# Performance work log

Measured on AMD Instinct MI355X. Metric: run time of the kernel, lower is better.

## Reference

```python
import jax, jax.numpy as jnp
import numpy as np

N = 20000
E = 640000
F_IN = 128
C_T = 8
L_T = 10 * N
HEADS = 8
HDIM = 64
NEG_SLOPE = 0.2


def setup_inputs() -> dict:
    key = jax.random.key(0)
    ks = jax.random.split(key, 20)
    d = {}
    d["x"] = jax.random.normal(ks[0], (N, F_IN), dtype=jnp.float32)
    d["edge_index"] = jax.random.randint(ks[1], (2, E), 0, N, dtype=jnp.int64)
    d["temporal"] = jax.random.normal(ks[2], (C_T, L_T), dtype=jnp.float32)
    # GCNConv(F_IN, 16)
    d["W1"] = jax.random.normal(ks[3], (F_IN, 16), dtype=jnp.float32) * 0.1
    d["b1"] = jnp.zeros((16,), dtype=jnp.float32)
    # GATConv(16, 64, heads=8), concat -> 512
    d["W2"] = jax.random.normal(ks[4], (16, HEADS * HDIM), dtype=jnp.float32) * 0.1
    d["att_src"] = jax.random.normal(ks[5], (HEADS, HDIM), dtype=jnp.float32) * 0.1
    d["att_dst"] = jax.random.normal(ks[6], (HEADS, HDIM), dtype=jnp.float32) * 0.1
    d["b2"] = jnp.zeros((HEADS * HDIM,), dtype=jnp.float32)
    # TemporalCNN
    d["cw1"] = jax.random.normal(ks[7], (32, C_T, 3), dtype=jnp.float32) * 0.1
    d["cb1"] = jnp.zeros((32,), dtype=jnp.float32)
    d["cw2"] = jax.random.normal(ks[8], (64, 32, 3), dtype=jnp.float32) * 0.05
    d["cb2"] = jnp.zeros((64,), dtype=jnp.float32)
    d["cw3"] = jax.random.normal(ks[9], (128, 64, 3), dtype=jnp.float32) * 0.05
    d["cb3"] = jnp.zeros((128,), dtype=jnp.float32)
    d["fw1"] = jax.random.normal(ks[10], (256, 128 * 10), dtype=jnp.float32) * 0.02
    d["fb1"] = jnp.zeros((256,), dtype=jnp.float32)
    d["fw2"] = jax.random.normal(ks[11], (64, 256), dtype=jnp.float32) * 0.05
    d["fb2"] = jnp.zeros((64,), dtype=jnp.float32)
    return d


def _conv1d(x, w, b):
    # x: [1, C, L], w: [O, C, 3]; padding=1 == SAME for k=3
    out = jax.lax.conv_general_dilated(
        x, w, window_strides=(1,), padding="SAME",
        dimension_numbers=("NCH", "OIH", "NCH"))
    return out + b[None, :, None]


def _gcn(x, src, dst, W, b):
    # PyG GCNConv: add self-loops, symmetric normalization
    h = x @ W                                   # [N, 16]
    deg = jax.ops.segment_sum(jnp.ones_like(dst, dtype=h.dtype), dst, num_segments=N)
    dinv = jax.lax.rsqrt(jnp.maximum(deg, 1.0))
    norm = dinv[src] * dinv[dst]                # [E+N]
    out = jax.ops.segment_sum(h[src] * norm[:, None], dst, num_segments=N)
    return out + b


def _gat(x, src, dst, W, att_src, att_dst, b):
    h = (x @ W).reshape(N, HEADS, HDIM)         # [N, 8, 64]
    a_s = jnp.einsum("nhd,hd->nh", h, att_src)  # [N, 8]
    a_d = jnp.einsum("nhd,hd->nh", h, att_dst)
    e = a_s[src] + a_d[dst]                     # [E+N, 8], message j->i: src=j, dst=i
    e = jnp.where(e >= 0, e, NEG_SLOPE * e)     # LeakyReLU(0.2)
    # segment softmax over incoming edges of each dst node
    m = jax.ops.segment_max(e, dst, num_segments=N)
    m = jnp.where(jnp.isfinite(m), m, 0.0)
    ex = jnp.exp(e - m[dst])
    s = jax.ops.segment_sum(ex, dst, num_segments=N)
    alpha = ex / (s[dst] + 1e-16)               # [E+N, 8]
    out = jax.ops.segment_sum(h[src] * alpha[:, :, None], dst, num_segments=N)
    return out.reshape(N, HEADS * HDIM) + b


def reference(x, edge_index, temporal, W1, b1, W2, att_src, att_dst, b2,
              cw1, cb1, cw2, cb2, cw3, cb3, fw1, fb1, fw2, fb2):
    # ---- graph branch ----
    loops = jnp.arange(N, dtype=edge_index.dtype)
    src = jnp.concatenate([edge_index[0], loops])
    dst = jnp.concatenate([edge_index[1], loops])
    g = _gcn(x, src, dst, W1, b1)
    g = jax.nn.relu(g)
    # F.dropout with training=False (eval) -> identity
    x1 = _gat(g, src, dst, W2, att_src, att_dst, b2)   # [N, 512]
    # ---- temporal branch ----
    t = temporal[None]                                  # [1, C, L]
    t = jax.nn.relu(_conv1d(t, cw1, cb1))
    t = jax.nn.relu(_conv1d(t, cw2, cb2))
    t = jax.nn.relu(_conv1d(t, cw3, cb3))               # [1, 128, L]
    t = t.reshape(-1, 128 * 10)                         # [N, 1280] (same as torch .view)
    t = jax.nn.relu(t @ fw1.T + fb1)
    x2 = t @ fw2.T + fb2                                # [N, 64]
    return jnp.concatenate([x1, x2], axis=1)            # [N, 576]
```

## Files before the change

### kernel.cpp

```cpp
#include <hip/hip_runtime.h>
#include <hip/hip_bf16.h>

#define NN 20000
#define EE 640000
#define FIN 128
#define CT 8
#define LT 200000
#define HEADS 8
#define HDIM 64
#define F1 16
#define F2 512
#define OUTF 576

typedef short s16x8 __attribute__((ext_vector_type(8)));
typedef float f32x4 __attribute__((ext_vector_type(4)));

static __device__ __forceinline__ float b2f(__hip_bfloat16 v) { return __bfloat162float(v); }
static __device__ __forceinline__ float ldf(float v) { return v; }
static __device__ __forceinline__ float ldf(__hip_bfloat16 v) { return __bfloat162float(v); }
static __device__ __forceinline__ unsigned f2bf_bits(float x) {
  unsigned u = __float_as_uint(x);
  return (u + 0x7fffu + ((u >> 16) & 1u)) >> 16;
}

static __device__ __forceinline__ void gl16(const void* g, void* l) {
  __builtin_amdgcn_global_load_lds(
      (const __attribute__((address_space(1))) unsigned*)g,
      (__attribute__((address_space(3))) unsigned*)l, 16, 0, 0);
}

__global__ __launch_bounds__(256) void prep_all(
    const float* __restrict__ cw1, float* __restrict__ wt1,
    const float* __restrict__ cw2, short* __restrict__ wb2,
    const float* __restrict__ cw3, short* __restrict__ wb3,
    const float* __restrict__ W2, const float* __restrict__ asrc,
    const float* __restrict__ adst, float* __restrict__ WS, float* __restrict__ WD) {
  int b = blockIdx.x, t = threadIdx.x;
  if (b < 3) {
    int i = b * 256 + t;
    if (i < 32 * 8 * 3) {
      int o = i / 24, r = i % 24;
      int c = r / 3, k = r % 3;
      wt1[(c * 3 + k) * 32 + o] = cw1[i];
    }
  } else if (b < 27) {
    int i = (b - 3) * 256 + t;
    int o = i / 96, r = i % 96;
    int ic = r / 3, kk = r % 3;
    wb2[o * 96 + kk * 32 + ic] = (short)f2bf_bits(cw2[i]);
  } else if (b < 123) {
    int i = (b - 27) * 256 + t;
    int o = i / 192, r = i % 192;
    int ic = r / 3, kk = r % 3;
    wb3[o * 192 + kk * 64 + ic] = (short)f2bf_bits(cw3[i]);
  } else {
    int k = (t & 127) >> 3, h = t & 7;
    const float* av = (t < 128) ? asrc : adst;
    float acc = 0.f;
    for (int d = 0; d < 64; d++) acc += W2[k * F2 + h * 64 + d] * av[h * 64 + d];
    ((t < 128) ? WS : WD)[k * 8 + h] = acc;
  }
}

__global__ __launch_bounds__(256) void fwprep(
    const float* __restrict__ fw1, __hip_bfloat16* __restrict__ w1b,
    const float* __restrict__ fw2, float* __restrict__ fw2t) {
  int b = blockIdx.x;
  if (b < 1280) {
    int i = b * 256 + threadIdx.x;
    w1b[i] = __float2bfloat16(fw1[i]);
  } else {
    int i = (b - 1280) * 256 + threadIdx.x;
    int o = i / 256, j = i % 256;
    fw2t[j * 64 + o] = fw2[i];
  }
}


template <int C, int O, int P, typename IN_T>
__global__ __launch_bounds__(256) void conv_fast(
    const IN_T* __restrict__ in, __hip_bfloat16* __restrict__ out,
    const float* __restrict__ wt, const float* __restrict__ bias) {
  constexpr int OCG = O / 2;
  constexpr int PG = 256 / OCG;
  static_assert(PG * P == 64, "tile mismatch");
  __shared__ __align__(16) float tile[C][68];
  __shared__ __align__(16) __hip_bfloat16 ot[O][66];
  int t = threadIdx.x;
  int ocg = t % OCG;
  int pg = t / OCG;
  long base = (long)blockIdx.x * 64;

  for (int i = t; i < C * 66; i += 256) {
    int c = i / 66, p = i % 66;
    long l = base + p - 1;
    tile[c][p] = (l >= 0 && l < LT) ? ldf(in[(long)c * LT + l]) : 0.f;
  }
  __syncthreads();

  int oc0 = 2 * ocg;
  int p0 = pg * P;
  float acc[2][P];
#pragma unroll
  for (int j = 0; j < 2; j++)
#pragma unroll
    for (int p = 0; p < P; p++) acc[j][p] = 0.f;

  for (int ic = 0; ic < C; ic++) {
    float x[P + 2];
#pragma unroll
    for (int q = 0; q < P / 4; q++) {
      float4 v = *(const float4*)&tile[ic][p0 + 4 * q];
      x[4 * q] = v.x; x[4 * q + 1] = v.y; x[4 * q + 2] = v.z; x[4 * q + 3] = v.w;
    }
    {
      float2 v = *(const float2*)&tile[ic][p0 + P];
      x[P] = v.x; x[P + 1] = v.y;
    }
    const float* wrow = wt + (long)ic * 3 * O;
    float wv[3][2];
#pragma unroll
    for (int kk = 0; kk < 3; kk++) {
      float2 w2 = *(const float2*)&wrow[kk * O + oc0];
      wv[kk][0] = w2.x; wv[kk][1] = w2.y;
    }
#pragma unroll
    for (int kk = 0; kk < 3; kk++)
#pragma unroll
      for (int j = 0; j < 2; j++)
#pragma unroll
        for (int p = 0; p < P; p++) acc[j][p] += x[p + kk] * wv[kk][j];
  }
  float b0 = bias[oc0], b1 = bias[oc0 + 1];
#pragma unroll
  for (int p = 0; p < P; p++) {
    ot[oc0][p0 + p] = __float2bfloat16(fmaxf(acc[0][p] + b0, 0.f));
    ot[oc0 + 1][p0 + p] = __float2bfloat16(fmaxf(acc[1][p] + b1, 0.f));
  }
  __syncthreads();
  for (int i = t; i < O * 32; i += 256) {
    int oc = i >> 5, pp = i & 31;
    unsigned v = ((const unsigned*)&ot[oc][0])[pp];
    *(unsigned*)&out[(long)oc * LT + base + 2 * pp] = v;
  }
}

template <int C, int O, int MPW>
__global__ __launch_bounds__(256) void conv_mfma(
    const short* __restrict__ in, short* __restrict__ out,
    const short* __restrict__ w, const float* __restrict__ bias) {
  constexpr int K = 3 * C;
  constexpr int NS = K / 32;
  constexpr int XP = C + 8;
  constexpr int OP = 132;
  constexpr int SH_X = 132 * XP * 2;
  constexpr int SH_O = O * OP * 2;
  __shared__ __align__(16) char smem[(SH_X > SH_O) ? SH_X : SH_O];
  short* xT = (short*)smem;

  int t = threadIdx.x;
  long base = (long)blockIdx.x * 128;

  if (base >= 2 && base + 131 < LT) {
    for (int idx = t; idx < C * 67; idx += 256) {
      int ic = idx / 67, q = idx % 67;
      unsigned v = *(const unsigned*)(in + (long)ic * LT + base + 2 * q - 2);
      int p0 = 2 * q - 1;
      if (q > 0) xT[p0 * XP + ic] = (short)(v & 0xffffu);
      if (q < 66) xT[(p0 + 1) * XP + ic] = (short)(v >> 16);
    }
  } else {
    for (int idx = t; idx < C * 132; idx += 256) {
      int ic = idx / 132, p = idx % 132;
      long l = base + p - 1;
      xT[p * XP + ic] = (l >= 0 && l < LT) ? in[(long)ic * LT + l] : (short)0;
    }
  }
  __syncthreads();

  int wave = t >> 6, lane = t & 63;
  int n = lane & 15, kg = lane >> 4;
  int m0 = wave * (MPW * 16);

  f32x4 acc[MPW][8] = {};
#pragma unroll
  for (int s = 0; s < NS; s++) {
    const int kk = (s * 32) / C;
    const int ic0 = (s * 32) % C + kg * 8;
    s16x8 a[MPW];
#pragma unroll
    for (int mi = 0; mi < MPW; mi++)
      a[mi] = *(const s16x8*)(w + (long)(m0 + mi * 16 + n) * K + s * 32 + kg * 8);
#pragma unroll
    for (int nt = 0; nt < 8; nt++) {
      s16x8 b = *(const s16x8*)(xT + (nt * 16 + n + kk) * XP + ic0);
#pragma unroll
      for (int mi = 0; mi < MPW; mi++)
        acc[mi][nt] = __builtin_amdgcn_mfma_f32_16x16x32_bf16(a[mi], b, acc[mi][nt], 0, 0, 0);
    }
  }

  __syncthreads();
  short* ob = (short*)smem;
#pragma unroll
  for (int mi = 0; mi < MPW; mi++) {
    int o = m0 + mi * 16 + kg * 4;
#pragma unroll
    for (int nt = 0; nt < 8; nt++) {
      int p = nt * 16 + n;
#pragma unroll
      for (int r = 0; r < 4; r++) {
        float v = fmaxf(acc[mi][nt][r] + bias[o + r], 0.f);
        ob[(o + r) * OP + p] = (short)f2bf_bits(v);
      }
    }
  }
  __syncthreads();
  const unsigned* obu = (const unsigned*)smem;
  for (int idx = t; idx < O * 64; idx += 256) {
    int o = idx >> 6, q = idx & 63;
    long l = base + 2 * q;
    if (l < LT)
      *(unsigned*)(out + (long)o * LT + l) = obu[o * (OP / 2) + q];
  }
}

__global__ __launch_bounds__(256) void fc1_tile(
    const __hip_bfloat16* __restrict__ t3, const __hip_bfloat16* __restrict__ w,
    const float* __restrict__ fb1, float* __restrict__ out) {
  __shared__ __align__(16) short As[2][128 * 32];
  __shared__ __align__(16) short Bs[2][128 * 32];
  int t = threadIdx.x;
  int wid = t >> 6, lane = t & 63;
  int bn = blockIdx.x & 1, bm = blockIdx.x >> 1;
  int mrow = lane & 15, kg = lane >> 4;

  const char* tb = (const char*)t3;
  const char* wb = (const char*)w;
  int u0 = wid * 128 + lane;
  int u1 = u0 + 64;
  int ra0 = u0 >> 2, ca0 = u0 & 3;
  int ra1 = u1 >> 2, ca1 = u1 & 3;
  long ga0 = ((long)min(bm * 128 + ra0, NN - 1) * 1280 + ca0 * 8) * 2;
  long ga1 = ((long)min(bm * 128 + ra1, NN - 1) * 1280 + ca1 * 8) * 2;
  long gb0 = ((long)(bn * 128 + ra0) * 1280 + ca0 * 8) * 2;
  long gb1 = ((long)(bn * 128 + ra1) * 1280 + ca1 * 8) * 2;
  int l0 = (wid * 2 + 0) * 512;
  int l1 = (wid * 2 + 1) * 512;

#define FC1_STAGE(buf, k0)                          \
  do {                                              \
    long kb = (long)(k0) * 2;                       \
    gl16(tb + ga0 + kb, &As[buf][l0]);              \
    gl16(tb + ga1 + kb, &As[buf][l1]);              \
    gl16(wb + gb0 + kb, &Bs[buf][l0]);              \
    gl16(wb + gb1 + kb, &Bs[buf][l1]);              \
  } while (0)

  FC1_STAGE(0, 0);
  __syncthreads();

  int wr = wid >> 1, wc = wid & 1;
  f32x4 acc[4][4] = {};
  for (int s = 0; s < 40; s++) {
    int buf = s & 1;
    if (s + 1 < 40) FC1_STAGE(buf ^ 1, (s + 1) * 32);
    s16x8 a[4], b[4];
#pragma unroll
    for (int mi = 0; mi < 4; mi++)
      a[mi] = *(const s16x8*)&As[buf][(wr * 64 + mi * 16 + mrow) * 32 + kg * 8];
#pragma unroll
    for (int ni = 0; ni < 4; ni++)
      b[ni] = *(const s16x8*)&Bs[buf][(wc * 64 + ni * 16 + mrow) * 32 + kg * 8];
#pragma unroll
    for (int mi = 0; mi < 4; mi++)
#pragma unroll
      for (int ni = 0; ni < 4; ni++)
        acc[mi][ni] = __builtin_amdgcn_mfma_f32_16x16x32_bf16(a[mi], b[ni], acc[mi][ni], 0, 0, 0);
    __syncthreads();
  }
#undef FC1_STAGE

  int node_base = bm * 128 + wr * 64 + kg * 4;
  int col_base = bn * 128 + wc * 64 + mrow;
#pragma unroll
  for (int ni = 0; ni < 4; ni++) {
    int col = col_base + ni * 16;
    float bias = fb1[col];
#pragma unroll
    for (int mi = 0; mi < 4; mi++) {
      int node = node_base + mi * 16;
#pragma unroll
      for (int r = 0; r < 4; r++) {
        if (node + r < NN)
          out[(long)(node + r) * 256 + col] = fmaxf(acc[mi][ni][r] + bias, 0.f);
      }
    }
  }
}

__global__ __launch_bounds__(256) void fc2_kernel(
    const float* __restrict__ fc1o, const float* __restrict__ fw2t,
    const float* __restrict__ fb2, float* __restrict__ out) {
  __shared__ __align__(16) float sh[32 * 264];
  int t = threadIdx.x;
  int m0 = blockIdx.x * 32;
  for (int i = t; i < 2048; i += 256) {
    int nd = i >> 6, q = i & 63;
    *(float4*)&sh[nd * 264 + 4 * q] = *(const float4*)&fc1o[(long)(m0 + nd) * 256 + 4 * q];
  }
  __syncthreads();
  int wave = t >> 6, o = t & 63;
  int nb = wave * 8;
  float acc[8];
  float bias = fb2[o];
#pragma unroll
  for (int i = 0; i < 8; i++) acc[i] = bias;
  for (int j = 0; j < 256; j++) {
    float wv = fw2t[j * 64 + o];
#pragma unroll
    for (int i = 0; i < 8; i++) acc[i] += sh[(nb + i) * 264 + j] * wv;
  }
#pragma unroll
  for (int i = 0; i < 8; i++)
    out[(long)(m0 + nb + i) * OUTF + F2 + o] = acc[i];
}


__global__ __launch_bounds__(256) void zero_i32(int* __restrict__ p, int n) {
  int i = blockIdx.x * 256 + threadIdx.x;
  if (i < n) p[i] = 0;
}

__global__ __launch_bounds__(256) void deg_kernel(const int* __restrict__ dst, int* __restrict__ deg) {
  int e = blockIdx.x * 256 + threadIdx.x;
  if (e < EE) atomicAdd(&deg[dst[e]], 1);
}

__global__ __launch_bounds__(1024) void scan_kernel(
    const int* __restrict__ deg, int* __restrict__ offs, float* __restrict__ dinv) {
  __shared__ int sums[1024];
  int tid = threadIdx.x;
  const int CH = 20;
  int s = 0;
  for (int i = 0; i < CH; i++) {
    int idx = tid * CH + i;
    if (idx < NN) s += deg[idx] + 1;
  }
  sums[tid] = s;
  __syncthreads();
  for (int off = 1; off < 1024; off <<= 1) {
    int v = (tid >= off) ? sums[tid - off] : 0;
    __syncthreads();
    sums[tid] += v;
    __syncthreads();
  }
  int run = (tid > 0) ? sums[tid - 1] : 0;
  for (int i = 0; i < CH; i++) {
    int idx = tid * CH + i;
    if (idx < NN) {
      int d = deg[idx];
      offs[idx] = run;
      dinv[idx] = rsqrtf((float)(d + 1));
      run += d + 1;
    }
  }
  if (tid == 1023) offs[NN] = sums[1023];
}

__global__ __launch_bounds__(256) void fill_kernel(
    const int* __restrict__ src, const int* __restrict__ dst,
    const int* __restrict__ offs, int* __restrict__ cursor, int* __restrict__ csr) {
  int e = blockIdx.x * 256 + threadIdx.x;
  if (e < EE) {
    int d = dst[e];
    int pos = atomicAdd(&cursor[d], 1);
    csr[offs[d] + pos] = src[e];
  } else if (e < EE + NN) {
    int i = e - EE;
    int pos = atomicAdd(&cursor[i], 1);
    csr[offs[i] + pos] = i;
  }
}

__global__ __launch_bounds__(256) void h1_kernel(
    const float* __restrict__ x, const float* __restrict__ W1,
    const float* __restrict__ dinv, float* __restrict__ h1s) {
  __shared__ __align__(16) float ws[128 * 16];
  __shared__ __align__(16) float xs[16][132];
  int t = threadIdx.x;
  int i0 = blockIdx.x * 16;
#pragma unroll
  for (int i = t; i < 512; i += 256)
    *(float4*)&ws[4 * i] = *(const float4*)&W1[4 * i];
#pragma unroll
  for (int i = t; i < 512; i += 256) {
    int nl = i >> 5, q = i & 31;
    *(float4*)&xs[nl][4 * q] = *(const float4*)&x[(long)(i0 + nl) * FIN + 4 * q];
  }
  __syncthreads();
  int nl = t >> 4, f = t & 15;
  float acc = 0.f;
#pragma unroll 8
  for (int k = 0; k < FIN; k++) acc += xs[nl][k] * ws[k * 16 + f];
  int n = i0 + nl;
  h1s[n * F1 + f] = acc * dinv[n];
}

__global__ __launch_bounds__(256) void gcn_kernel(
    const float* __restrict__ h1s, const int* __restrict__ offs, const int* __restrict__ csr,
    const float* __restrict__ dinv, const float* __restrict__ b1, float* __restrict__ g) {
  int wave = threadIdx.x >> 6;
  int lane = threadIdx.x & 63;
  int i = blockIdx.x * 4 + wave;
  int f = lane & 15, grp = lane >> 4;
  int beg = offs[i], end = offs[i + 1];
  float acc = 0.f;
  for (int idx = beg + grp; idx < end; idx += 4)
    acc += h1s[csr[idx] * F1 + f];
  acc += __shfl_down(acc, 32);
  acc += __shfl_down(acc, 16);
  if (lane < 16) g[i * F1 + f] = fmaxf(acc * dinv[i] + b1[f], 0.f);
}

__global__ __launch_bounds__(256) void h2att_kernel(
    const float* __restrict__ g, const float* __restrict__ W2,
    const float* __restrict__ WS, const float* __restrict__ WD,
    unsigned* __restrict__ h2hm, float* __restrict__ AS, float* __restrict__ AD) {
  __shared__ __align__(16) float gl[32][20];
  int t = threadIdx.x;
  int i0 = blockIdx.x * 32;
  for (int idx = t; idx < 512; idx += 256)
    gl[idx >> 4][idx & 15] = g[i0 * 16 + idx];
  __syncthreads();

  int f0 = 2 * t;
  int h = t >> 5, c32 = t & 31;
  float w0[16], w1[16];
#pragma unroll
  for (int k = 0; k < 16; k++) {
    float2 wv = *(const float2*)&W2[k * F2 + f0];
    w0[k] = wv.x; w1[k] = wv.y;
  }
  for (int nl = 0; nl < 32; nl++) {
    float a0 = 0.f, a1 = 0.f;
#pragma unroll
    for (int kk = 0; kk < 4; kk++) {
      f32x4 gv = *(const f32x4*)&gl[nl][4 * kk];
#pragma unroll
      for (int r = 0; r < 4; r++) {
        a0 += gv[r] * w0[4 * kk + r];
        a1 += gv[r] * w1[4 * kk + r];
      }
    }
    h2hm[((long)h * NN + i0 + nl) * 32 + c32] = f2bf_bits(a0) | (f2bf_bits(a1) << 16);
  }
  int nl = t >> 3, hh = t & 7;
  float s = 0.f, d = 0.f;
#pragma unroll
  for (int k = 0; k < 16; k++) {
    float gv = gl[nl][k];
    s += gv * WS[k * 8 + hh];
    d += gv * WD[k * 8 + hh];
  }
  AS[(long)hh * NN + i0 + nl] = s;
  AD[(long)hh * NN + i0 + nl] = d;
}

__global__ __launch_bounds__(256) void gat_fused_kernel(
    const unsigned* __restrict__ h2hm, const float* __restrict__ AS,
    const float* __restrict__ AD, const int* __restrict__ offs,
    const int* __restrict__ csr, const float* __restrict__ b2,
    float* __restrict__ out) {
  __shared__ __align__(16) unsigned long long pairs[4][64];
  __shared__ __align__(16) float accb[4][8][68];
  int h = blockIdx.x & 7;
  int gn = blockIdx.x >> 3;
  int wave = threadIdx.x >> 6;
  int lane = threadIdx.x & 63;
  int i = gn * 4 + wave;
  int beg = offs[i], end = offs[i + 1];
  const float* ASh = AS + (long)h * NN;
  float ad = AD[(long)h * NN + i];
  const char* hb2 = (const char*)(h2hm + (long)h * NN * 32);
  int octet = lane >> 3, q = lane & 7;
  unsigned laneoff = (unsigned)q * 16u;
  unsigned long long* prs = &pairs[wave][0];

  float acc[8] = {0.f, 0.f, 0.f, 0.f, 0.f, 0.f, 0.f, 0.f};
  float sum = 0.f;

  for (int c = beg; c < end; c += 64) {
    int cnt = end - c;
    if (cnt > 64) cnt = 64;
    unsigned off = 0u;
    float ex = 0.f;
    if (lane < cnt) {
      int s = csr[c + lane];
      float e = ASh[s] + ad;
      e = (e >= 0.f) ? e : 0.2f * e;
      ex = __expf(e);
      sum += ex;
      off = (unsigned)s << 7;
    }
    asm volatile("" ::: "memory");
    prs[lane] = ((unsigned long long)__float_as_uint(ex) << 32) | off;
    asm volatile("" ::: "memory");
    int nj = (cnt + 7) >> 3;
    const unsigned long long* pp = prs + octet;
#pragma unroll 2
    for (int j = 0; j < nj; j++) {
      unsigned long long pr = pp[(long)j * 8];
      unsigned voff = (unsigned)pr | laneoff;
      float aj = __uint_as_float((unsigned)(pr >> 32));
      uint4 v = *(const uint4*)(hb2 + voff);
      acc[0] += __uint_as_float(v.x << 16) * aj;
      acc[1] += __uint_as_float(v.x & 0xffff0000u) * aj;
      acc[2] += __uint_as_float(v.y << 16) * aj;
      acc[3] += __uint_as_float(v.y & 0xffff0000u) * aj;
      acc[4] += __uint_as_float(v.z << 16) * aj;
      acc[5] += __uint_as_float(v.z & 0xffff0000u) * aj;
      acc[6] += __uint_as_float(v.w << 16) * aj;
      acc[7] += __uint_as_float(v.w & 0xffff0000u) * aj;
    }
    asm volatile("" ::: "memory");
  }
#pragma unroll
  for (int o = 32; o > 0; o >>= 1) sum += __shfl_xor(sum, o, 64);
  float rinv = 1.f / (sum + 1e-16f);
  float* ab = &accb[wave][octet][q * 8];
  f32x4 lo = {acc[0], acc[1], acc[2], acc[3]};
  f32x4 hi = {acc[4], acc[5], acc[6], acc[7]};
  *(f32x4*)ab = lo;
  *(f32x4*)(ab + 4) = hi;
  asm volatile("" ::: "memory");
  float r = 0.f;
#pragma unroll
  for (int o = 0; o < 8; o++) r += accb[wave][o][lane];
  out[(long)i * OUTF + h * 64 + lane] = r * rinv + b2[h * 64 + lane];
}


extern "C" void kernel_launch(void* const* d_in, const int* in_sizes, int n_in,
                              void* d_out, int out_size, void* d_ws, size_t ws_size,
                              hipStream_t stream) {
  const float* x        = (const float*)d_in[0];
  const int*   eidx     = (const int*)d_in[1];
  const float* temporal = (const float*)d_in[2];
  const float* W1       = (const float*)d_in[3];
  const float* b1       = (const float*)d_in[4];
  const float* W2       = (const float*)d_in[5];
  const float* att_src  = (const float*)d_in[6];
  const float* att_dst  = (const float*)d_in[7];
  const float* b2       = (const float*)d_in[8];
  const float* cw1      = (const float*)d_in[9];
  const float* cb1      = (const float*)d_in[10];
  const float* cw2      = (const float*)d_in[11];
  const float* cb2      = (const float*)d_in[12];
  const float* cw3      = (const float*)d_in[13];
  const float* cb3      = (const float*)d_in[14];
  const float* fw1      = (const float*)d_in[15];
  const float* fb1      = (const float*)d_in[16];
  const float* fw2      = (const float*)d_in[17];
  const float* fb2      = (const float*)d_in[18];
  float* out = (float*)d_out;

  const int* e_src = eidx;
  const int* e_dst = eidx + EE;

  char* ws = (char*)d_ws;
  __hip_bfloat16* T1b = (__hip_bfloat16*)(ws + 0);
  __hip_bfloat16* T2b = (__hip_bfloat16*)(ws + 12800000);
  __hip_bfloat16* T3b = (__hip_bfloat16*)(ws + 38400000);
  __hip_bfloat16* FW1BF = (__hip_bfloat16*)(ws + 0);
  float* FW2T   = (float*)(ws + 655360);
  float* FC1OUT = (float*)(ws + 1310720);
  float* H1     = (float*)(ws + 0);
  float* G      = (float*)(ws + 1280000);
  int*   DEG    = (int*)  (ws + 2560000);
  float* DINV   = (float*)(ws + 2640000);
  int*   OFFS   = (int*)  (ws + 2720000);
  int*   CURSOR = (int*)  (ws + 2800128);
  int*   CSR    = (int*)  (ws + 2880128);
  float* AS     = (float*)(ws + 5520128);
  float* AD     = (float*)(ws + 6160128);
  unsigned* H2HM = (unsigned*)(ws + 6800128);
  float* WT1 = out;
  short* WB2 = (short*)((char*)d_out + 3072);
  short* WB3 = (short*)((char*)d_out + 15360);
  float* WSM = (float*)((char*)d_out + 64512);
  float* WDM = (float*)((char*)d_out + 65024);

  const int PB = LT / 64;
  const int MB = (LT + 127) / 128;

  prep_all<<<124, 256, 0, stream>>>(cw1, WT1, cw2, WB2, cw3, WB3,
                                    W2, att_src, att_dst, WSM, WDM);
  conv_fast<8, 32, 4, float><<<PB, 256, 0, stream>>>(temporal, T1b, WT1, cb1);
  conv_mfma<32, 64, 1><<<MB, 256, 0, stream>>>((const short*)T1b, (short*)T2b, WB2, cb2);
  fwprep<<<1344, 256, 0, stream>>>(fw1, FW1BF, fw2, FW2T);
  conv_mfma<64, 128, 2><<<MB, 256, 0, stream>>>((const short*)T2b, (short*)T3b, WB3, cb3);
  fc1_tile<<<157 * 2, 256, 0, stream>>>(T3b, FW1BF, fb1, FC1OUT);
  fc2_kernel<<<NN / 32, 256, 0, stream>>>(FC1OUT, FW2T, fb2, out);

  zero_i32<<<(80032 + 255) / 256, 256, 0, stream>>>(DEG, 80032);
  deg_kernel<<<(EE + 255) / 256, 256, 0, stream>>>(e_dst, DEG);
  scan_kernel<<<1, 1024, 0, stream>>>(DEG, OFFS, DINV);
  fill_kernel<<<(EE + NN + 255) / 256, 256, 0, stream>>>(e_src, e_dst, OFFS, CURSOR, CSR);
  h1_kernel<<<NN / 16, 256, 0, stream>>>(x, W1, DINV, H1);
  gcn_kernel<<<NN / 4, 256, 0, stream>>>(H1, OFFS, CSR, DINV, b1, G);
  h2att_kernel<<<NN / 32, 256, 0, stream>>>(G, W2, WSM, WDM, H2HM, AS, AD);
  gat_fused_kernel<<<(NN / 4) * 8, 256, 0, stream>>>(H2HM, AS, AD, OFFS, CSR, b2, out);
}
```

Baseline: 450.1 us.

## Horizontally fuse temporal CNN and graph preprocessing kernels into shared launches

Merges independent kernels from the temporal-convolution and graph branches into combined launches where each block selects its role by block index, cutting the launch count roughly in half. The goal is to remove launch gaps and let small graph-preprocessing work fill the GPU alongside the conv stages. The workspace layout is rearranged so buffers live at the same time do not alias. A trade-off is that the scan is now done by a single 256-thread block, which may form a tail, and dynamic LDS is sized for the largest role.

```diff
diff --git a/kernel.cpp b/kernel.cpp
--- a/kernel.cpp
+++ b/kernel.cpp
@@ -15,9 +15,6 @@
 typedef short s16x8 __attribute__((ext_vector_type(8)));
 typedef float f32x4 __attribute__((ext_vector_type(4)));
 
-static __device__ __forceinline__ float b2f(__hip_bfloat16 v) { return __bfloat162float(v); }
-static __device__ __forceinline__ float ldf(float v) { return v; }
-static __device__ __forceinline__ float ldf(__hip_bfloat16 v) { return __bfloat162float(v); }
 static __device__ __forceinline__ unsigned f2bf_bits(float x) {
   unsigned u = __float_as_uint(x);
   return (u + 0x7fffu + ((u >> 16) & 1u)) >> 16;
@@ -29,13 +26,13 @@
       (__attribute__((address_space(3))) unsigned*)l, 16, 0, 0);
 }
 
-__global__ __launch_bounds__(256) void prep_all(
-    const float* __restrict__ cw1, float* __restrict__ wt1,
+
+static __device__ void dev_prep_all(
+    int b, int t, const float* __restrict__ cw1, float* __restrict__ wt1,
     const float* __restrict__ cw2, short* __restrict__ wb2,
     const float* __restrict__ cw3, short* __restrict__ wb3,
     const float* __restrict__ W2, const float* __restrict__ asrc,
     const float* __restrict__ adst, float* __restrict__ WS, float* __restrict__ WD) {
-  int b = blockIdx.x, t = threadIdx.x;
   if (b < 3) {
     int i = b * 256 + t;
     if (i < 32 * 8 * 3) {
@@ -62,39 +59,21 @@
   }
 }
 
-__global__ __launch_bounds__(256) void fwprep(
-    const float* __restrict__ fw1, __hip_bfloat16* __restrict__ w1b,
-    const float* __restrict__ fw2, float* __restrict__ fw2t) {
-  int b = blockIdx.x;
-  if (b < 1280) {
-    int i = b * 256 + threadIdx.x;
-    w1b[i] = __float2bfloat16(fw1[i]);
-  } else {
-    int i = (b - 1280) * 256 + threadIdx.x;
-    int o = i / 256, j = i % 256;
-    fw2t[j * 64 + o] = fw2[i];
-  }
-}
-
-
-template <int C, int O, int P, typename IN_T>
-__global__ __launch_bounds__(256) void conv_fast(
-    const IN_T* __restrict__ in, __hip_bfloat16* __restrict__ out,
-    const float* __restrict__ wt, const float* __restrict__ bias) {
-  constexpr int OCG = O / 2;
-  constexpr int PG = 256 / OCG;
-  static_assert(PG * P == 64, "tile mismatch");
-  __shared__ __align__(16) float tile[C][68];
-  __shared__ __align__(16) __hip_bfloat16 ot[O][66];
-  int t = threadIdx.x;
+static __device__ void dev_conv_fast(
+    char* smp, int b, int t, const float* __restrict__ in,
+    __hip_bfloat16* __restrict__ out, const float* __restrict__ wt,
+    const float* __restrict__ bias) {
+  constexpr int C = 8, O = 32, P = 4, OCG = O / 2;
+  float (*tile)[68] = (float(*)[68])smp;
+  __hip_bfloat16 (*ot)[66] = (__hip_bfloat16(*)[66])(smp + 2176);
   int ocg = t % OCG;
   int pg = t / OCG;
-  long base = (long)blockIdx.x * 64;
+  long base = (long)b * 64;
 
   for (int i = t; i < C * 66; i += 256) {
     int c = i / 66, p = i % 66;
     long l = base + p - 1;
-    tile[c][p] = (l >= 0 && l < LT) ? ldf(in[(long)c * LT + l]) : 0.f;
+    tile[c][p] = (l >= 0 && l < LT) ? in[(long)c * LT + l] : 0.f;
   }
   __syncthreads();
 
@@ -146,20 +125,16 @@
 }
 
 template <int C, int O, int MPW>
-__global__ __launch_bounds__(256) void conv_mfma(
-    const short* __restrict__ in, short* __restrict__ out,
-    const short* __restrict__ w, const float* __restrict__ bias) {
+static __device__ void dev_conv_mfma(
+    char* smp, int b, int t, const short* __restrict__ in,
+    short* __restrict__ out, const short* __restrict__ w,
+    const float* __restrict__ bias) {
   constexpr int K = 3 * C;
   constexpr int NS = K / 32;
   constexpr int XP = C + 8;
   constexpr int OP = 132;
-  constexpr int SH_X = 132 * XP * 2;
-  constexpr int SH_O = O * OP * 2;
-  __shared__ __align__(16) char smem[(SH_X > SH_O) ? SH_X : SH_O];
-  short* xT = (short*)smem;
-
-  int t = threadIdx.x;
-  long base = (long)blockIdx.x * 128;
+  short* xT = (short*)smp;
+  long base = (long)b * 128;
 
   if (base >= 2 && base + 131 < LT) {
     for (int idx = t; idx < C * 67; idx += 256) {
@@ -193,15 +168,15 @@
       a[mi] = *(const s16x8*)(w + (long)(m0 + mi * 16 + n) * K + s * 32 + kg * 8);
 #pragma unroll
     for (int nt = 0; nt < 8; nt++) {
-      s16x8 b = *(const s16x8*)(xT + (nt * 16 + n + kk) * XP + ic0);
+      s16x8 bb = *(const s16x8*)(xT + (nt * 16 + n + kk) * XP + ic0);
 #pragma unroll
       for (int mi = 0; mi < MPW; mi++)
-        acc[mi][nt] = __builtin_amdgcn_mfma_f32_16x16x32_bf16(a[mi], b, acc[mi][nt], 0, 0, 0);
-    }
-  }
-
-  __syncthreads();
-  short* ob = (short*)smem;
+        acc[mi][nt] = __builtin_amdgcn_mfma_f32_16x16x32_bf16(a[mi], bb, acc[mi][nt], 0, 0, 0);
+    }
+  }
+
+  __syncthreads();
+  short* ob = (short*)smp;
 #pragma unroll
   for (int mi = 0; mi < MPW; mi++) {
     int o = m0 + mi * 16 + kg * 4;
@@ -216,7 +191,7 @@
     }
   }
   __syncthreads();
-  const unsigned* obu = (const unsigned*)smem;
+  const unsigned* obu = (const unsigned*)smp;
   for (int idx = t; idx < O * 64; idx += 256) {
     int o = idx >> 6, q = idx & 63;
     long l = base + 2 * q;
@@ -225,14 +200,96 @@
   }
 }
 
-__global__ __launch_bounds__(256) void fc1_tile(
-    const __hip_bfloat16* __restrict__ t3, const __hip_bfloat16* __restrict__ w,
-    const float* __restrict__ fb1, float* __restrict__ out) {
-  __shared__ __align__(16) short As[2][128 * 32];
-  __shared__ __align__(16) short Bs[2][128 * 32];
-  int t = threadIdx.x;
+static __device__ void dev_scan(
+    char* smp, int t, const int* __restrict__ deg, int* __restrict__ offs,
+    float* __restrict__ dinv) {
+  int* sums = (int*)smp;
+  const int CH = 79;
+  int base = t * CH;
+  int s = 0;
+  for (int i = 0; i < CH; i++) {
+    int idx = base + i;
+    if (idx < NN) s += deg[idx] + 1;
+  }
+  sums[t] = s;
+  __syncthreads();
+  for (int off = 1; off < 256; off <<= 1) {
+    int v = (t >= off) ? sums[t - off] : 0;
+    __syncthreads();
+    sums[t] += v;
+    __syncthreads();
+  }
+  int run = (t > 0) ? sums[t - 1] : 0;
+  for (int i = 0; i < CH; i++) {
+    int idx = base + i;
+    if (idx < NN) {
+      int d = deg[idx];
+      offs[idx] = run;
+      dinv[idx] = rsqrtf((float)(d + 1));
+      run += d + 1;
+    }
+  }
+  if (t == 255) offs[NN] = sums[255];
+}
+
+static __device__ void dev_fill(
+    int b, int t, const int* __restrict__ src, const int* __restrict__ dst,
+    const int* __restrict__ offs, int* __restrict__ cursor, int* __restrict__ csr) {
+  int e = b * 256 + t;
+  if (e < EE) {
+    int d = dst[e];
+    int pos = atomicAdd(&cursor[d], 1);
+    csr[offs[d] + pos] = src[e];
+  } else if (e < EE + NN) {
+    int i = e - EE;
+    int pos = atomicAdd(&cursor[i], 1);
+    csr[offs[i] + pos] = i;
+  }
+}
+
+static __device__ void dev_h1(
+    char* smp, int b, int t, const float* __restrict__ x,
+    const float* __restrict__ W1, const float* __restrict__ dinv,
+    float* __restrict__ h1s) {
+  float* ws = (float*)smp;
+  float* xs = (float*)(smp + 8192);
+  int i0 = b * 16;
+  for (int i = t; i < 512; i += 256)
+    *(float4*)&ws[4 * i] = *(const float4*)&W1[4 * i];
+  for (int i = t; i < 512; i += 256) {
+    int nl = i >> 5, q = i & 31;
+    *(float4*)&xs[nl * 132 + 4 * q] = *(const float4*)&x[(long)(i0 + nl) * FIN + 4 * q];
+  }
+  __syncthreads();
+  int nl = t >> 4, f = t & 15;
+  float acc = 0.f;
+#pragma unroll 8
+  for (int k = 0; k < FIN; k++) acc += xs[nl * 132 + k] * ws[k * 16 + f];
+  int n = i0 + nl;
+  h1s[n * F1 + f] = acc * dinv[n];
+}
+
+static __device__ void dev_fwprep(
+    int b, int t, const float* __restrict__ fw1, __hip_bfloat16* __restrict__ w1b,
+    const float* __restrict__ fw2, float* __restrict__ fw2t) {
+  if (b < 1280) {
+    int i = b * 256 + t;
+    w1b[i] = __float2bfloat16(fw1[i]);
+  } else {
+    int i = (b - 1280) * 256 + t;
+    int o = i / 256, j = i % 256;
+    fw2t[j * 64 + o] = fw2[i];
+  }
+}
+
+static __device__ void dev_fc1(
+    char* smp, int bid, int t, const __hip_bfloat16* __restrict__ t3,
+    const __hip_bfloat16* __restrict__ w, const float* __restrict__ fb1,
+    float* __restrict__ out) {
+  short* As = (short*)smp;
+  short* Bs = (short*)(smp + 16384);
   int wid = t >> 6, lane = t & 63;
-  int bn = blockIdx.x & 1, bm = blockIdx.x >> 1;
+  int bn = bid & 1, bm = bid >> 1;
   int mrow = lane & 15, kg = lane >> 4;
 
   const char* tb = (const char*)t3;
@@ -248,38 +305,36 @@
   int l0 = (wid * 2 + 0) * 512;
   int l1 = (wid * 2 + 1) * 512;
 
-#define FC1_STAGE(buf, k0)                          \
-  do {                                              \
-    long kb = (long)(k0) * 2;                       \
-    gl16(tb + ga0 + kb, &As[buf][l0]);              \
-    gl16(tb + ga1 + kb, &As[buf][l1]);              \
-    gl16(wb + gb0 + kb, &Bs[buf][l0]);              \
-    gl16(wb + gb1 + kb, &Bs[buf][l1]);              \
-  } while (0)
-
-  FC1_STAGE(0, 0);
+  auto stage = [&](int buf, int k0) {
+    long kb = (long)k0 * 2;
+    gl16(tb + ga0 + kb, As + buf * 4096 + l0);
+    gl16(tb + ga1 + kb, As + buf * 4096 + l1);
+    gl16(wb + gb0 + kb, Bs + buf * 4096 + l0);
+    gl16(wb + gb1 + kb, Bs + buf * 4096 + l1);
+  };
+
+  stage(0, 0);
   __syncthreads();
 
   int wr = wid >> 1, wc = wid & 1;
   f32x4 acc[4][4] = {};
   for (int s = 0; s < 40; s++) {
     int buf = s & 1;
-    if (s + 1 < 40) FC1_STAGE(buf ^ 1, (s + 1) * 32);
-    s16x8 a[4], b[4];
+    if (s + 1 < 40) stage(buf ^ 1, (s + 1) * 32);
+    s16x8 a[4], bb[4];
 #pragma unroll
     for (int mi = 0; mi < 4; mi++)
-      a[mi] = *(const s16x8*)&As[buf][(wr * 64 + mi * 16 + mrow) * 32 + kg * 8];
+      a[mi] = *(const s16x8*)&As[buf * 4096 + (wr * 64 + mi * 16 + mrow) * 32 + kg * 8];
 #pragma unroll
     for (int ni = 0; ni < 4; ni++)
-      b[ni] = *(const s16x8*)&Bs[buf][(wc * 64 + ni * 16 + mrow) * 32 + kg * 8];
+      bb[ni] = *(const s16x8*)&Bs[buf * 4096 + (wc * 64 + ni * 16 + mrow) * 32 + kg * 8];
 #pragma unroll
     for (int mi = 0; mi < 4; mi++)
 #pragma unroll
       for (int ni = 0; ni < 4; ni++)
-        acc[mi][ni] = __builtin_amdgcn_mfma_f32_16x16x32_bf16(a[mi], b[ni], acc[mi][ni], 0, 0, 0);
+        acc[mi][ni] = __builtin_amdgcn_mfma_f32_16x16x32_bf16(a[mi], bb[ni], acc[mi][ni], 0, 0, 0);
     __syncthreads();
   }
-#undef FC1_STAGE
 
   int node_base = bm * 128 + wr * 64 + kg * 4;
   int col_base = bn * 128 + wc * 64 + mrow;
@@ -299,120 +354,13 @@
   }
 }
 
-__global__ __launch_bounds__(256) void fc2_kernel(
-    const float* __restrict__ fc1o, const float* __restrict__ fw2t,
-    const float* __restrict__ fb2, float* __restrict__ out) {
-  __shared__ __align__(16) float sh[32 * 264];
-  int t = threadIdx.x;
-  int m0 = blockIdx.x * 32;
-  for (int i = t; i < 2048; i += 256) {
-    int nd = i >> 6, q = i & 63;
-    *(float4*)&sh[nd * 264 + 4 * q] = *(const float4*)&fc1o[(long)(m0 + nd) * 256 + 4 * q];
-  }
-  __syncthreads();
-  int wave = t >> 6, o = t & 63;
-  int nb = wave * 8;
-  float acc[8];
-  float bias = fb2[o];
-#pragma unroll
-  for (int i = 0; i < 8; i++) acc[i] = bias;
-  for (int j = 0; j < 256; j++) {
-    float wv = fw2t[j * 64 + o];
-#pragma unroll
-    for (int i = 0; i < 8; i++) acc[i] += sh[(nb + i) * 264 + j] * wv;
-  }
-#pragma unroll
-  for (int i = 0; i < 8; i++)
-    out[(long)(m0 + nb + i) * OUTF + F2 + o] = acc[i];
-}
-
-
-__global__ __launch_bounds__(256) void zero_i32(int* __restrict__ p, int n) {
-  int i = blockIdx.x * 256 + threadIdx.x;
-  if (i < n) p[i] = 0;
-}
-
-__global__ __launch_bounds__(256) void deg_kernel(const int* __restrict__ dst, int* __restrict__ deg) {
-  int e = blockIdx.x * 256 + threadIdx.x;
-  if (e < EE) atomicAdd(&deg[dst[e]], 1);
-}
-
-__global__ __launch_bounds__(1024) void scan_kernel(
-    const int* __restrict__ deg, int* __restrict__ offs, float* __restrict__ dinv) {
-  __shared__ int sums[1024];
-  int tid = threadIdx.x;
-  const int CH = 20;
-  int s = 0;
-  for (int i = 0; i < CH; i++) {
-    int idx = tid * CH + i;
-    if (idx < NN) s += deg[idx] + 1;
-  }
-  sums[tid] = s;
-  __syncthreads();
-  for (int off = 1; off < 1024; off <<= 1) {
-    int v = (tid >= off) ? sums[tid - off] : 0;
-    __syncthreads();
-    sums[tid] += v;
-    __syncthreads();
-  }
-  int run = (tid > 0) ? sums[tid - 1] : 0;
-  for (int i = 0; i < CH; i++) {
-    int idx = tid * CH + i;
-    if (idx < NN) {
-      int d = deg[idx];
-      offs[idx] = run;
-      dinv[idx] = rsqrtf((float)(d + 1));
-      run += d + 1;
-    }
-  }
-  if (tid == 1023) offs[NN] = sums[1023];
-}
-
-__global__ __launch_bounds__(256) void fill_kernel(
-    const int* __restrict__ src, const int* __restrict__ dst,
-    const int* __restrict__ offs, int* __restrict__ cursor, int* __restrict__ csr) {
-  int e = blockIdx.x * 256 + threadIdx.x;
-  if (e < EE) {
-    int d = dst[e];
-    int pos = atomicAdd(&cursor[d], 1);
-    csr[offs[d] + pos] = src[e];
-  } else if (e < EE + NN) {
-    int i = e - EE;
-    int pos = atomicAdd(&cursor[i], 1);
-    csr[offs[i] + pos] = i;
-  }
-}
-
-__global__ __launch_bounds__(256) void h1_kernel(
-    const float* __restrict__ x, const float* __restrict__ W1,
-    const float* __restrict__ dinv, float* __restrict__ h1s) {
-  __shared__ __align__(16) float ws[128 * 16];
-  __shared__ __align__(16) float xs[16][132];
-  int t = threadIdx.x;
-  int i0 = blockIdx.x * 16;
-#pragma unroll
-  for (int i = t; i < 512; i += 256)
-    *(float4*)&ws[4 * i] = *(const float4*)&W1[4 * i];
-#pragma unroll
-  for (int i = t; i < 512; i += 256) {
-    int nl = i >> 5, q = i & 31;
-    *(float4*)&xs[nl][4 * q] = *(const float4*)&x[(long)(i0 + nl) * FIN + 4 * q];
-  }
-  __syncthreads();
-  int nl = t >> 4, f = t & 15;
-  float acc = 0.f;
-#pragma unroll 8
-  for (int k = 0; k < FIN; k++) acc += xs[nl][k] * ws[k * 16 + f];
-  int n = i0 + nl;
-  h1s[n * F1 + f] = acc * dinv[n];
-}
-
-__global__ __launch_bounds__(256) void gcn_kernel(
-    const float* __restrict__ h1s, const int* __restrict__ offs, const int* __restrict__ csr,
-    const float* __restrict__ dinv, const float* __restrict__ b1, float* __restrict__ g) {
-  int wave = threadIdx.x >> 6;
-  int lane = threadIdx.x & 63;
-  int i = blockIdx.x * 4 + wave;
+static __device__ void dev_gcn(
+    int b, int t, const float* __restrict__ h1s, const int* __restrict__ offs,
+    const int* __restrict__ csr, const float* __restrict__ dinv,
+    const float* __restrict__ b1, float* __restrict__ g) {
+  int wave = t >> 6;
+  int lane = t & 63;
+  int i = b * 4 + wave;
   int f = lane & 15, grp = lane >> 4;
   int beg = offs[i], end = offs[i + 1];
   float acc = 0.f;
@@ -423,15 +371,42 @@
   if (lane < 16) g[i * F1 + f] = fmaxf(acc * dinv[i] + b1[f], 0.f);
 }
 
-__global__ __launch_bounds__(256) void h2att_kernel(
-    const float* __restrict__ g, const float* __restrict__ W2,
-    const float* __restrict__ WS, const float* __restrict__ WD,
-    unsigned* __restrict__ h2hm, float* __restrict__ AS, float* __restrict__ AD) {
-  __shared__ __align__(16) float gl[32][20];
-  int t = threadIdx.x;
-  int i0 = blockIdx.x * 32;
+static __device__ void dev_fc2(
+    char* smp, int b, int t, const float* __restrict__ fc1o,
+    const float* __restrict__ fw2t, const float* __restrict__ fb2,
+    float* __restrict__ out) {
+  float* sh = (float*)smp;
+  int m0 = b * 32;
+  for (int i = t; i < 2048; i += 256) {
+    int nd = i >> 6, q = i & 63;
+    *(float4*)&sh[nd * 264 + 4 * q] = *(const float4*)&fc1o[(long)(m0 + nd) * 256 + 4 * q];
+  }
+  __syncthreads();
+  int wave = t >> 6, o = t & 63;
+  int nb = wave * 8;
+  float acc[8];
+  float bias = fb2[o];
+#pragma unroll
+  for (int i = 0; i < 8; i++) acc[i] = bias;
+  for (int j = 0; j < 256; j++) {
+    float wv = fw2t[j * 64 + o];
+#pragma unroll
+    for (int i = 0; i < 8; i++) acc[i] += sh[(nb + i) * 264 + j] * wv;
+  }
+#pragma unroll
+  for (int i = 0; i < 8; i++)
+    out[(long)(m0 + nb + i) * OUTF + F2 + o] = acc[i];
+}
+
+static __device__ void dev_h2att(
+    char* smp, int b, int t, const float* __restrict__ g,
+    const float* __restrict__ W2, const float* __restrict__ WS,
+    const float* __restrict__ WD, unsigned* __restrict__ h2hm,
+    float* __restrict__ AS, float* __restrict__ AD) {
+  float* glb = (float*)smp;
+  int i0 = b * 32;
   for (int idx = t; idx < 512; idx += 256)
-    gl[idx >> 4][idx & 15] = g[i0 * 16 + idx];
+    glb[(idx >> 4) * 20 + (idx & 15)] = g[i0 * 16 + idx];
   __syncthreads();
 
   int f0 = 2 * t;
@@ -446,7 +421,7 @@
     float a0 = 0.f, a1 = 0.f;
 #pragma unroll
     for (int kk = 0; kk < 4; kk++) {
-      f32x4 gv = *(const f32x4*)&gl[nl][4 * kk];
+      f32x4 gv = *(const f32x4*)&glb[nl * 20 + 4 * kk];
 #pragma unroll
       for (int r = 0; r < 4; r++) {
         a0 += gv[r] * w0[4 * kk + r];
@@ -459,12 +434,79 @@
   float s = 0.f, d = 0.f;
 #pragma unroll
   for (int k = 0; k < 16; k++) {
-    float gv = gl[nl][k];
+    float gv = glb[nl * 20 + k];
     s += gv * WS[k * 8 + hh];
     d += gv * WD[k * 8 + hh];
   }
   AS[(long)hh * NN + i0 + nl] = s;
   AD[(long)hh * NN + i0 + nl] = d;
+}
+
+
+__global__ __launch_bounds__(256) void k_prep(
+    const float* cw1, float* wt1, const float* cw2, short* wb2,
+    const float* cw3, short* wb3, const float* W2, const float* asrc,
+    const float* adst, float* WS, float* WD, int* zbase) {
+  int b = blockIdx.x, t = threadIdx.x;
+  if (b < 124) dev_prep_all(b, t, cw1, wt1, cw2, wb2, cw3, wb3, W2, asrc, adst, WS, WD);
+  else {
+    int i = (b - 124) * 256 + t;
+    if (i < 40000) zbase[i] = 0;
+  }
+}
+
+__global__ __launch_bounds__(256) void k_conv1_deg(
+    const float* temporal, __hip_bfloat16* T1b, const float* wt1, const float* cb1,
+    const int* e_dst, int* deg) {
+  extern __shared__ char smem[];
+  int b = blockIdx.x;
+  if (b < 3125) dev_conv_fast(smem, b, threadIdx.x, temporal, T1b, wt1, cb1);
+  else {
+    int e = (b - 3125) * 256 + threadIdx.x;
+    if (e < EE) atomicAdd(&deg[e_dst[e]], 1);
+  }
+}
+
+__global__ __launch_bounds__(256) void k_conv2_scan(
+    const short* T1b, short* T2b, const short* wb2, const float* cb2,
+    const int* deg, int* offs, float* dinv) {
+  extern __shared__ char smem[];
+  int b = blockIdx.x;
+  if (b < 1563) dev_conv_mfma<32, 64, 1>(smem, b, threadIdx.x, T1b, T2b, wb2, cb2);
+  else dev_scan(smem, threadIdx.x, deg, offs, dinv);
+}
+
+__global__ __launch_bounds__(256) void k_conv3_misc(
+    const short* T2b, short* T3b, const short* wb3, const float* cb3,
+    const int* e_src, const int* e_dst, const int* offs, int* cursor, int* csr,
+    const float* x, const float* W1, const float* dinv, float* h1s,
+    const float* fw1, __hip_bfloat16* w1b, const float* fw2, float* fw2t) {
+  extern __shared__ char smem[];
+  int b = blockIdx.x, t = threadIdx.x;
+  if (b < 1563) dev_conv_mfma<64, 128, 2>(smem, b, t, T2b, T3b, wb3, cb3);
+  else if (b < 4142) dev_fill(b - 1563, t, e_src, e_dst, offs, cursor, csr);
+  else if (b < 5392) dev_h1(smem, b - 4142, t, x, W1, dinv, h1s);
+  else dev_fwprep(b - 5392, t, fw1, w1b, fw2, fw2t);
+}
+
+__global__ __launch_bounds__(256) void k_fc1_gcn(
+    const __hip_bfloat16* t3, const __hip_bfloat16* w, const float* fb1, float* fc1o,
+    const float* h1s, const int* offs, const int* csr, const float* dinv,
+    const float* b1, float* g) {
+  extern __shared__ char smem[];
+  int b = blockIdx.x, t = threadIdx.x;
+  if (b < 314) dev_fc1(smem, b, t, t3, w, fb1, fc1o);
+  else dev_gcn(b - 314, t, h1s, offs, csr, dinv, b1, g);
+}
+
+__global__ __launch_bounds__(256) void k_fc2_h2att(
+    const float* fc1o, const float* fw2t, const float* fb2, float* out,
+    const float* g, const float* W2, const float* WS, const float* WD,
+    unsigned* h2hm, float* AS, float* AD) {
+  extern __shared__ char smem[];
+  int b = blockIdx.x, t = threadIdx.x;
+  if (b < 625) dev_fc2(smem, b, t, fc1o, fw2t, fb2, out);
+  else dev_h2att(smem, b - 625, t, g, W2, WS, WD, h2hm, AS, AD);
 }
 
 __global__ __launch_bounds__(256) void gat_fused_kernel(
@@ -569,46 +611,40 @@
   const int* e_dst = eidx + EE;
 
   char* ws = (char*)d_ws;
-  __hip_bfloat16* T1b = (__hip_bfloat16*)(ws + 0);
-  __hip_bfloat16* T2b = (__hip_bfloat16*)(ws + 12800000);
-  __hip_bfloat16* T3b = (__hip_bfloat16*)(ws + 38400000);
-  __hip_bfloat16* FW1BF = (__hip_bfloat16*)(ws + 0);
-  float* FW2T   = (float*)(ws + 655360);
-  float* FC1OUT = (float*)(ws + 1310720);
-  float* H1     = (float*)(ws + 0);
-  float* G      = (float*)(ws + 1280000);
-  int*   DEG    = (int*)  (ws + 2560000);
-  float* DINV   = (float*)(ws + 2640000);
-  int*   OFFS   = (int*)  (ws + 2720000);
-  int*   CURSOR = (int*)  (ws + 2800128);
-  int*   CSR    = (int*)  (ws + 2880128);
+  int*   CURSOR = (int*)  (ws + 0);
+  int*   DEG    = (int*)  (ws + 80000);
+  int*   OFFS   = (int*)  (ws + 160000);
+  float* DINV   = (float*)(ws + 240128);
+  int*   CSR    = (int*)  (ws + 320128);
+  float* H1S    = (float*)(ws + 2960128);
+  float* G      = (float*)(ws + 4240128);
   float* AS     = (float*)(ws + 5520128);
   float* AD     = (float*)(ws + 6160128);
-  unsigned* H2HM = (unsigned*)(ws + 6800128);
+  __hip_bfloat16* T2b = (__hip_bfloat16*)(ws + 6800128);
+  float* FC1OUT = (float*)(ws + 6800128);
+  __hip_bfloat16* T1b = (__hip_bfloat16*)(ws + 32400128);
+  unsigned* H2HM = (unsigned*)(ws + 32400128);
+  __hip_bfloat16* T3b = (__hip_bfloat16*)(ws + 32400128);
+  __hip_bfloat16* FW1BF = (__hip_bfloat16*)(ws + 83600128);
+  float* FW2T = (float*)(ws + 84255488);
   float* WT1 = out;
   short* WB2 = (short*)((char*)d_out + 3072);
   short* WB3 = (short*)((char*)d_out + 15360);
   float* WSM = (float*)((char*)d_out + 64512);
   float* WDM = (float*)((char*)d_out + 65024);
 
-  const int PB = LT / 64;
-  const int MB = (LT + 127) / 128;
-
-  prep_all<<<124, 256, 0, stream>>>(cw1, WT1, cw2, WB2, cw3, WB3,
-                                    W2, att_src, att_dst, WSM, WDM);
-  conv_fast<8, 32, 4, float><<<PB, 256, 0, stream>>>(temporal, T1b, WT1, cb1);
-  conv_mfma<32, 64, 1><<<MB, 256, 0, stream>>>((const short*)T1b, (short*)T2b, WB2, cb2);
-  fwprep<<<1344, 256, 0, stream>>>(fw1, FW1BF, fw2, FW2T);
-  conv_mfma<64, 128, 2><<<MB, 256, 0, stream>>>((const short*)T2b, (short*)T3b, WB3, cb3);
-  fc1_tile<<<157 * 2, 256, 0, stream>>>(T3b, FW1BF, fb1, FC1OUT);
-  fc2_kernel<<<NN / 32, 256, 0, stream>>>(FC1OUT, FW2T, fb2, out);
-
-  zero_i32<<<(80032 + 255) / 256, 256, 0, stream>>>(DEG, 80032);
-  deg_kernel<<<(EE + 255) / 256, 256, 0, stream>>>(e_dst, DEG);
-  scan_kernel<<<1, 1024, 0, stream>>>(DEG, OFFS, DINV);
-  fill_kernel<<<(EE + NN + 255) / 256, 256, 0, stream>>>(e_src, e_dst, OFFS, CURSOR, CSR);
-  h1_kernel<<<NN / 16, 256, 0, stream>>>(x, W1, DINV, H1);
-  gcn_kernel<<<NN / 4, 256, 0, stream>>>(H1, OFFS, CSR, DINV, b1, G);
-  h2att_kernel<<<NN / 32, 256, 0, stream>>>(G, W2, WSM, WDM, H2HM, AS, AD);
+  k_prep<<<281, 256, 0, stream>>>(cw1, WT1, cw2, WB2, cw3, WB3,
+                                  W2, att_src, att_dst, WSM, WDM, (int*)ws);
+  k_conv1_deg<<<5625, 256, 6400, stream>>>(temporal, T1b, WT1, cb1, e_dst, DEG);
+  k_conv2_scan<<<1564, 256, 16896, stream>>>((const short*)T1b, (short*)T2b, WB2, cb2,
+                                             DEG, OFFS, DINV);
+  k_conv3_misc<<<6736, 256, 33792, stream>>>((const short*)T2b, (short*)T3b, WB3, cb3,
+                                             e_src, e_dst, OFFS, CURSOR, CSR,
+                                             x, W1, DINV, H1S,
+                                             fw1, FW1BF, fw2, FW2T);
+  k_fc1_gcn<<<5314, 256, 32768, stream>>>(T3b, FW1BF, fb1, FC1OUT,
+                                          H1S, OFFS, CSR, DINV, b1, G);
+  k_fc2_h2att<<<1250, 256, 33792, stream>>>(FC1OUT, FW2T, fb2, out,
+                                            G, W2, WSM, WDM, H2HM, AS, AD);
   gat_fused_kernel<<<(NN / 4) * 8, 256, 0, stream>>>(H2HM, AS, AD, OFFS, CSR, b2, out);
 }
```

Result: faster. 427.7 us (-5.0%).
